# Kernel tuning notes

Measured on AMD Instinct MI355X. Metric: run time of the kernel, lower is better.

The kernel has to match this reference:

```python
import jax, jax.numpy as jnp
import numpy as np

N = 100000
NFEAT = 128
NHID = 16
HEADS = 8
NCLASS = 40
E = 1600000
NEG_SLOPE = 0.2  # PyG GATConv default


def glorot(key, shape):
    fan = shape[0] + shape[-1]
    limit = float(np.sqrt(6.0 / fan))
    return jax.random.uniform(key, shape, jnp.float32, -limit, limit)


def setup_inputs() -> dict:
    key = jax.random.key(0)
    ks = jax.random.split(key, 10)
    x = jax.random.normal(ks[0], (N, NFEAT), jnp.float32)
    adj = jnp.zeros((1,), jnp.float32)  # unused by forward, kept for signature parity
    edge_index = jax.random.randint(ks[1], (2, E), 0, N, jnp.int64)
    # layer 1: GATConv(NFEAT, NHID, heads=HEADS)
    W1 = glorot(ks[2], (NFEAT, HEADS * NHID))
    att_src1 = glorot(ks[3], (HEADS, NHID))
    att_dst1 = glorot(ks[4], (HEADS, NHID))
    b1 = jnp.zeros((HEADS * NHID,), jnp.float32)
    # layer 2: GATConv(HEADS*NHID, NCLASS, heads=1)
    W2 = glorot(ks[5], (HEADS * NHID, NCLASS))
    att_src2 = glorot(ks[6], (1, NCLASS))
    att_dst2 = glorot(ks[7], (1, NCLASS))
    b2 = jnp.zeros((NCLASS,), jnp.float32)
    return {"x": x, "adj": adj, "edge_index": edge_index,
            "W1": W1, "att_src1": att_src1, "att_dst1": att_dst1, "b1": b1,
            "W2": W2, "att_src2": att_src2, "att_dst2": att_dst2, "b2": b2}


def gat_conv(x, W, att_src, att_dst, bias, src, dst, heads, out_ch):
    n = x.shape[0]
    h = (x @ W).reshape(n, heads, out_ch)              # [N,H,C]
    a_src = (h * att_src[None]).sum(-1)                # [N,H]
    a_dst = (h * att_dst[None]).sum(-1)                # [N,H]
    e = jax.nn.leaky_relu(a_src[src] + a_dst[dst], NEG_SLOPE)  # [E,H]
    # softmax over incoming edges of each destination node
    m = jax.ops.segment_max(e, dst, num_segments=n)
    e = jnp.exp(e - m[dst])
    s = jax.ops.segment_sum(e, dst, num_segments=n)
    alpha = e / s[dst]                                  # [E,H]
    msg = h[src] * alpha[:, :, None]                    # [E,H,C]
    out = jax.ops.segment_sum(msg, dst, num_segments=n)  # [N,H,C]
    return out.reshape(n, heads * out_ch) + bias


def reference(x, adj, edge_index, W1, att_src1, att_dst1, b1, W2, att_src2, att_dst2, b2):
    # PyG GATConv adds self-loops by default
    loops = jnp.arange(N, dtype=edge_index.dtype)
    src = jnp.concatenate([edge_index[0], loops])
    dst = jnp.concatenate([edge_index[1], loops])
    # eval mode: F.dropout is identity
    h = jax.nn.elu(gat_conv(x, W1, att_src1, att_dst1, b1, src, dst, HEADS, NHID))
    h = jax.nn.elu(gat_conv(h, W2, att_src2, att_dst2, b2, src, dst, 1, NCLASS))
    return jax.nn.log_softmax(h, axis=1)
```

## Files before the change

kernel.cpp:

```cpp
#include <hip/hip_runtime.h>
#include <stdint.h>

#define NEG_SLOPE 0.2f

__device__ __forceinline__ float lrelu(float v) { return v >= 0.f ? v : NEG_SLOPE * v; }
__device__ __forceinline__ float elu(float v) { return v > 0.f ? v : expm1f(v); }
__device__ __forceinline__ float pexp(float v) { return __expf(lrelu(v)); }

typedef _Float16 h16x2 __attribute__((ext_vector_type(2)));
typedef _Float16 half8 __attribute__((ext_vector_type(8)));
typedef float floatx4 __attribute__((ext_vector_type(4)));

__device__ __forceinline__ void fma_h2(float& a0, float& a1, float p, unsigned u) {
    h16x2 h = __builtin_bit_cast(h16x2, u);
    a0 += p * (float)h[0];
    a1 += p * (float)h[1];
}


__global__ void zero_deg_kernel(int* __restrict__ deg, int n) {
    int t = blockIdx.x * blockDim.x + threadIdx.x;
    if (t < n) deg[t] = 0;
}

__global__ void hist_kernel(const int* __restrict__ ei, int* __restrict__ deg,
                            int* __restrict__ rank, int E, int n) {
    int e = blockIdx.x * blockDim.x + threadIdx.x;
    if (e >= E) return;
    int s = ei[e], d = ei[E + e];
    int r = -1;
    if ((unsigned)s < (unsigned)n && (unsigned)d < (unsigned)n)
        r = atomicAdd(&deg[d], 1);
    rank[e] = r;
}

#define SCAN_T 256
#define SCAN_TILE 1024

__global__ __launch_bounds__(SCAN_T) void scan_p1_kernel(const int* __restrict__ deg,
                                                         int* __restrict__ bsum, int n) {
    __shared__ int red[SCAN_T];
    int t = threadIdx.x;
    int base = blockIdx.x * SCAN_TILE + t * 4;
    int s = 0;
    #pragma unroll
    for (int i = 0; i < 4; i++) {
        int idx = base + i;
        if (idx < n) s += deg[idx];
    }
    red[t] = s;
    __syncthreads();
    for (int off = SCAN_T / 2; off; off >>= 1) {
        if (t < off) red[t] += red[t + off];
        __syncthreads();
    }
    if (t == 0) bsum[blockIdx.x] = red[0];
}

__global__ __launch_bounds__(1024) void scan_p2_kernel(int* __restrict__ bsum, int nb,
                                                       int* __restrict__ total) {
    __shared__ int sh[1024];
    int t = threadIdx.x;
    int v = (t < nb) ? bsum[t] : 0;
    sh[t] = v;
    __syncthreads();
    for (int off = 1; off < 1024; off <<= 1) {
        int add = (t >= off) ? sh[t - off] : 0;
        __syncthreads();
        sh[t] += add;
        __syncthreads();
    }
    if (t < nb) bsum[t] = sh[t] - v;
    if (t == nb - 1) *total = sh[t];
}

__global__ __launch_bounds__(SCAN_T) void scan_p3_kernel(const int* __restrict__ deg,
                                                         const int* __restrict__ bsum,
                                                         int* __restrict__ row_ptr, int n) {
    __shared__ int red[SCAN_T];
    int t = threadIdx.x;
    int base = blockIdx.x * SCAN_TILE + t * 4;
    int v[4];
    int s = 0;
    #pragma unroll
    for (int i = 0; i < 4; i++) {
        int idx = base + i;
        v[i] = (idx < n) ? deg[idx] : 0;
        s += v[i];
    }
    red[t] = s;
    __syncthreads();
    for (int off = 1; off < SCAN_T; off <<= 1) {
        int add = (t >= off) ? red[t - off] : 0;
        __syncthreads();
        red[t] += add;
        __syncthreads();
    }
    int excl = red[t] - s + bsum[blockIdx.x];
    #pragma unroll
    for (int i = 0; i < 4; i++) {
        int idx = base + i;
        if (idx < n) row_ptr[idx] = excl;
        excl += v[i];
    }
}

__global__ void scatter_kernel(const int* __restrict__ ei, const int* __restrict__ rank,
                               const int* __restrict__ row_ptr,
                               int* __restrict__ csr_src, int E, int n) {
    int e = blockIdx.x * blockDim.x + threadIdx.x;
    if (e >= E) return;
    int r = rank[e];
    if (r < 0) return;
    int s = ei[e], d = ei[E + e];
    csr_src[row_ptr[d] + r] = s;
}


__global__ void w1t_kernel(const float* __restrict__ W1, _Float16* __restrict__ w1t) {
    int t = blockIdx.x * 256 + threadIdx.x;
    int col = t >> 7, k = t & 127;
    w1t[col * 128 + k] = (_Float16)W1[k * 128 + col];
}

__global__ __launch_bounds__(256) void gemm1_mfma_kernel(
    const float* __restrict__ x, const _Float16* __restrict__ w1t,
    const float* __restrict__ as1, const float* __restrict__ ad1,
    _Float16* __restrict__ h1h, float* __restrict__ a1s, float* __restrict__ a1d, int n) {
    __shared__ __align__(16) char Wl[32768];
    const int tid = threadIdx.x;
    {
        const uint4* Wg = (const uint4*)w1t;
        #pragma unroll
        for (int i = 0; i < 8; i++) {
            int it = tid + i * 256;
            uint4 v = Wg[it];
            int b = it * 16;
            *(uint4*)&Wl[b ^ (((b >> 8) & 7) << 4)] = v;
        }
    }
    const int wave = tid >> 6, lane = tid & 63;
    const int cl = lane & 15, g = lane >> 4;
    const int wbase = blockIdx.x * 64 + wave * 16;

    int arow = wbase + cl;
    if (arow >= n) arow = n - 1;
    half8 afr[4];
    #pragma unroll
    for (int t = 0; t < 4; t++) {
        const float4 v0 = *(const float4*)&x[(size_t)arow * 128 + 32 * t + g * 8];
        const float4 v1 = *(const float4*)&x[(size_t)arow * 128 + 32 * t + g * 8 + 4];
        afr[t][0] = (_Float16)v0.x; afr[t][1] = (_Float16)v0.y;
        afr[t][2] = (_Float16)v0.z; afr[t][3] = (_Float16)v0.w;
        afr[t][4] = (_Float16)v1.x; afr[t][5] = (_Float16)v1.y;
        afr[t][6] = (_Float16)v1.z; afr[t][7] = (_Float16)v1.w;
    }
    __syncthreads();

    #pragma unroll
    for (int ct = 0; ct < 8; ct++) {
        const int col = ct * 16 + cl;
        half8 bfr[4];
        #pragma unroll
        for (int t = 0; t < 4; t++) {
            int b = (col << 8) + 64 * t + 16 * g;
            bfr[t] = *(half8*)&Wl[b ^ ((col & 7) << 4)];
        }
        floatx4 acc = {0.f, 0.f, 0.f, 0.f};
        #pragma unroll
        for (int t = 0; t < 4; t++)
            acc = __builtin_amdgcn_mfma_f32_16x16x32_f16(afr[t], bfr[t], acc, 0, 0, 0);
        const float av = as1[col], dv = ad1[col];
        #pragma unroll
        for (int i = 0; i < 4; i++) {
            int r = wbase + g * 4 + i;
            float hv = acc[i];
            if (r < n) h1h[(size_t)r * 128 + col] = (_Float16)hv;
            float ps = hv * av, pd = hv * dv;
            ps += __shfl_xor(ps, 1); ps += __shfl_xor(ps, 2);
            ps += __shfl_xor(ps, 4); ps += __shfl_xor(ps, 8);
            pd += __shfl_xor(pd, 1); pd += __shfl_xor(pd, 2);
            pd += __shfl_xor(pd, 4); pd += __shfl_xor(pd, 8);
            if (cl == 0 && r < n) {
                a1s[r * 8 + ct] = ps;
                a1d[r * 8 + ct] = pd;
            }
        }
    }
}

__global__ __launch_bounds__(256) void agg1_kernel(const int* __restrict__ row_ptr,
                                                   const int* __restrict__ csr_src,
                                                   const float* __restrict__ a1s,
                                                   const float* __restrict__ a1d,
                                                   const uint4* __restrict__ h1q,
                                                   const float* __restrict__ b1,
                                                   float* __restrict__ h2, int n) {
    int lane = threadIdx.x & 63;
    int d = blockIdx.x * 4 + (threadIdx.x >> 6);
    if (d >= n) return;
    const int g = lane >> 4;
    const int q = lane & 15;
    const int h = q >> 1;
    const float adh = a1d[d * 8 + h];

    float acc[8];
    #pragma unroll
    for (int i = 0; i < 8; i++) acc[i] = 0.f;
    float sum = 0.f;
    if (g == 0) {
        uint4 w = h1q[(size_t)d * 16 + q];
        float ps = pexp(a1s[d * 8 + h] + adh);
        fma_h2(acc[0], acc[1], ps, w.x);
        fma_h2(acc[2], acc[3], ps, w.y);
        fma_h2(acc[4], acc[5], ps, w.z);
        fma_h2(acc[6], acc[7], ps, w.w);
        sum = ps;
    }
    int beg = row_ptr[d], end = row_ptr[d + 1];
    for (int e = beg + g; e < end; e += 4) {
        int s = csr_src[e];
        uint4 w = h1q[(size_t)s * 16 + q];
        float p = pexp(a1s[s * 8 + h] + adh);
        fma_h2(acc[0], acc[1], p, w.x);
        fma_h2(acc[2], acc[3], p, w.y);
        fma_h2(acc[4], acc[5], p, w.z);
        fma_h2(acc[6], acc[7], p, w.w);
        sum += p;
    }
    sum += __shfl_xor(sum, 16); sum += __shfl_xor(sum, 32);
    #pragma unroll
    for (int i = 0; i < 8; i++) {
        acc[i] += __shfl_xor(acc[i], 16);
        acc[i] += __shfl_xor(acc[i], 32);
    }
    if (g == 0) {
        float rs = 1.f / sum;
        float4 b0 = *(const float4*)&b1[8 * q];
        float4 b4 = *(const float4*)&b1[8 * q + 4];
        float4 o0, o1;
        o0.x = elu(acc[0] * rs + b0.x); o0.y = elu(acc[1] * rs + b0.y);
        o0.z = elu(acc[2] * rs + b0.z); o0.w = elu(acc[3] * rs + b0.w);
        o1.x = elu(acc[4] * rs + b4.x); o1.y = elu(acc[5] * rs + b4.y);
        o1.z = elu(acc[6] * rs + b4.z); o1.w = elu(acc[7] * rs + b4.w);
        *(float4*)&h2[(size_t)d * 128 + 8 * q] = o0;
        *(float4*)&h2[(size_t)d * 128 + 8 * q + 4] = o1;
    }
}


#define WT_STRIDE 136
__global__ __launch_bounds__(320, 4) void gemm2_kernel(const float* __restrict__ h2,
                                                       const float* __restrict__ W2,
                                                       float* __restrict__ h3f,
                                                       _Float16* __restrict__ h3h,
                                                       int n) {
    __shared__ float WsT[40 * WT_STRIDE];
    __shared__ float xs[64][128];
    const int tid = threadIdx.x;
    const int j = tid % 40;
    const int no = tid / 40;
    const int base = blockIdx.x * 64;

    #pragma unroll 1
    for (int i = tid; i < 128 * 40; i += 320) {
        int k = i / 40, jj = i % 40;
        WsT[jj * WT_STRIDE + k] = W2[i];
    }
    #pragma unroll 1
    for (int q = tid; q < 64 * 32; q += 320) {
        int nn = q >> 5, c4 = q & 31;
        int node = base + nn;
        float4 v = make_float4(0.f, 0.f, 0.f, 0.f);
        if (node < n) v = *(const float4*)&h2[(size_t)node * 128 + c4 * 4];
        *(float4*)&xs[nn][c4 * 4] = v;
    }
    __syncthreads();

    float acc[8];
    #pragma unroll
    for (int m = 0; m < 8; m++) acc[m] = 0.f;
    #pragma unroll 4
    for (int k4 = 0; k4 < 128; k4 += 4) {
        float4 wv = *(const float4*)&WsT[j * WT_STRIDE + k4];
        #pragma unroll
        for (int m = 0; m < 8; m++) {
            float4 xv = *(const float4*)&xs[no + m * 8][k4];
            acc[m] += xv.x * wv.x + xv.y * wv.y + xv.z * wv.z + xv.w * wv.w;
        }
    }
    #pragma unroll
    for (int m = 0; m < 8; m++) {
        int node = base + no + m * 8;
        if (node < n) {
            h3f[(size_t)node * 40 + j] = acc[m];
            h3h[(size_t)node * 40 + j] = (_Float16)acc[m];
        }
    }
}

__global__ void attn2_kernel(const float* __restrict__ h3f, const float* __restrict__ as2,
                             const float* __restrict__ ad2,
                             float* __restrict__ a2s, float* __restrict__ a2d, int n) {
    int t = blockIdx.x * blockDim.x + threadIdx.x;
    if (t >= n) return;
    const float* row = &h3f[(size_t)t * 40];
    float ss = 0.f, dd = 0.f;
    #pragma unroll
    for (int c = 0; c < 40; c++) {
        float v = row[c];
        ss += v * as2[c];
        dd += v * ad2[c];
    }
    a2s[t] = ss;
    a2d[t] = dd;
}

__global__ __launch_bounds__(256) void agg2_final_kernel(const int* __restrict__ row_ptr,
                                                         const int* __restrict__ csr_src,
                                                         const float* __restrict__ a2s,
                                                         const float* __restrict__ a2d,
                                                         const float* __restrict__ h3f,
                                                         const unsigned* __restrict__ h3p,
                                                         const float* __restrict__ b2,
                                                         float* __restrict__ out, int n) {
    int lane = threadIdx.x & 63;
    int d = blockIdx.x * 4 + (threadIdx.x >> 6);
    if (d >= n) return;
    const int g = lane >> 5;
    const int q = lane & 31;
    const bool act = (q < 20);

    float2 hv = make_float2(0.f, 0.f);
    if (act && g == 0) hv = *(const float2*)&h3f[(size_t)d * 40 + 2 * q];
    const float adh = a2d[d];

    float acc0 = 0.f, acc1 = 0.f, sum = 0.f;
    if (g == 0) {
        float ps = pexp(a2s[d] + adh);
        acc0 = ps * hv.x; acc1 = ps * hv.y; sum = ps;
    }
    int beg = row_ptr[d], end = row_ptr[d + 1];
    int e = beg + g;
    for (; e + 6 < end; e += 8) {
        int s0 = csr_src[e],     s1 = csr_src[e + 2];
        int s2 = csr_src[e + 4], s3 = csr_src[e + 6];
        float a0 = a2s[s0], a1 = a2s[s1], a2 = a2s[s2], a3 = a2s[s3];
        unsigned w0 = 0u, w1 = 0u, w2 = 0u, w3 = 0u;
        if (act) {
            w0 = h3p[(size_t)s0 * 20 + q]; w1 = h3p[(size_t)s1 * 20 + q];
            w2 = h3p[(size_t)s2 * 20 + q]; w3 = h3p[(size_t)s3 * 20 + q];
        }
        float p0 = pexp(a0 + adh), p1 = pexp(a1 + adh);
        float p2 = pexp(a2 + adh), p3 = pexp(a3 + adh);
        fma_h2(acc0, acc1, p0, w0);
        fma_h2(acc0, acc1, p1, w1);
        fma_h2(acc0, acc1, p2, w2);
        fma_h2(acc0, acc1, p3, w3);
        sum += (p0 + p1) + (p2 + p3);
    }
    for (; e < end; e += 2) {
        int s = csr_src[e];
        float pe = pexp(a2s[s] + adh);
        unsigned w = act ? h3p[(size_t)s * 20 + q] : 0u;
        fma_h2(acc0, acc1, pe, w);
        sum += pe;
    }
    sum += __shfl_xor(sum, 32);
    acc0 += __shfl_xor(acc0, 32);
    acc1 += __shfl_xor(acc1, 32);

    float rs = 1.f / sum;
    float v0 = -3.0e38f, v1 = -3.0e38f;
    if (act) {
        v0 = elu(acc0 * rs + b2[2 * q]);
        v1 = elu(acc1 * rs + b2[2 * q + 1]);
    }
    float mx = (act && g == 0) ? fmaxf(v0, v1) : -3.0e38f;
    #pragma unroll
    for (int off = 32; off; off >>= 1) mx = fmaxf(mx, __shfl_xor(mx, off, 64));
    float es = (act && g == 0) ? (__expf(v0 - mx) + __expf(v1 - mx)) : 0.f;
    #pragma unroll
    for (int off = 32; off; off >>= 1) es += __shfl_xor(es, off, 64);
    if (act && g == 0) {
        float ls = logf(es);
        float2 o;
        o.x = v0 - mx - ls;
        o.y = v1 - mx - ls;
        *(float2*)&out[(size_t)d * 40 + 2 * q] = o;
    }
}

extern "C" void kernel_launch(void* const* d_in, const int* in_sizes, int n_in,
                              void* d_out, int out_size, void* d_ws, size_t ws_size,
                              hipStream_t stream) {
    const float* x   = (const float*)d_in[0];
    const int*   ei  = (const int*)d_in[2];
    const float* W1  = (const float*)d_in[3];
    const float* as1 = (const float*)d_in[4];
    const float* ad1 = (const float*)d_in[5];
    const float* b1  = (const float*)d_in[6];
    const float* W2  = (const float*)d_in[7];
    const float* as2 = (const float*)d_in[8];
    const float* ad2 = (const float*)d_in[9];
    const float* b2  = (const float*)d_in[10];
    float* out = (float*)d_out;

    const int n = in_sizes[0] / 128;
    const int E = in_sizes[2] / 2;
    const int nb = (n + SCAN_TILE - 1) / SCAN_TILE;

    float* ws = (float*)d_ws;
    _Float16* h1h = (_Float16*)ws;
    float* h2 = ws + (size_t)n * 64;
    float* A  = h2 + (size_t)n * 128;
    int* deg    = (int*)A;
    int* bsum   = deg + n;
    float* a1s  = A;
    float* a1d  = A + (size_t)n * 8;
    float* a2s  = A;
    float* a2d  = A + (size_t)n;
    int* row_ptr = (int*)(A + (size_t)n * 16);
    int* csr_src = row_ptr + (n + 1);
    int* rank    = csr_src + E;
    _Float16* w1t = (_Float16*)(((uintptr_t)(rank + E) + 63) & ~(uintptr_t)63);
    _Float16* h3h = h1h;
    float* h3f = ws + (size_t)n * 20;

    w1t_kernel<<<64, 256, 0, stream>>>(W1, w1t);
    zero_deg_kernel<<<(n + 255) / 256, 256, 0, stream>>>(deg, n);
    hist_kernel<<<(E + 255) / 256, 256, 0, stream>>>(ei, deg, rank, E, n);
    scan_p1_kernel<<<nb, SCAN_T, 0, stream>>>(deg, bsum, n);
    scan_p2_kernel<<<1, 1024, 0, stream>>>(bsum, nb, &row_ptr[n]);
    scan_p3_kernel<<<nb, SCAN_T, 0, stream>>>(deg, bsum, row_ptr, n);
    scatter_kernel<<<(E + 255) / 256, 256, 0, stream>>>(ei, rank, row_ptr, csr_src, E, n);

    gemm1_mfma_kernel<<<(n + 63) / 64, 256, 0, stream>>>(x, w1t, as1, ad1, h1h, a1s, a1d, n);
    agg1_kernel<<<(n + 3) / 4, 256, 0, stream>>>(row_ptr, csr_src, a1s, a1d,
                                                 (const uint4*)h1h, b1, h2, n);

    gemm2_kernel<<<(n + 63) / 64, 320, 0, stream>>>(h2, W2, h3f, h3h, n);
    attn2_kernel<<<(n + 255) / 256, 256, 0, stream>>>(h3f, as2, ad2, a2s, a2d, n);
    agg2_final_kernel<<<(n + 3) / 4, 256, 0, stream>>>(row_ptr, csr_src, a2s, a2d, h3f,
                                                       (const unsigned*)h3h, b2, out, n);
}
```

Before: 485.5 us.

## Use fp16 MFMA for layer-2 GEMM, fuse attention scores, store h2 as fp16

Layer-1 aggregation now writes its ELU output as fp16 instead of fp32. Layer 2 then runs its projection with 16x16x32 f16 MFMA instructions against a pre-transposed, zero-padded fp16 W2, and computes the attention source and destination scores in the same kernel, which removes the separate attn2 pass. The agg1 edge loop is also unrolled by two to keep more gathers in flight. The aim is to cut h2 memory traffic and FP32 FMA cost in gemm2, at the price of fp16 rounding of the layer-2 input.

Result: faster. 419.3 us (-13.6%).

```diff
diff --git a/kernel.cpp b/kernel.cpp
--- a/kernel.cpp
+++ b/kernel.cpp
@@ -122,6 +122,14 @@
     int col = t >> 7, k = t & 127;
     w1t[col * 128 + k] = (_Float16)W1[k * 128 + col];
 }
+
+__global__ void w2t_kernel(const float* __restrict__ W2, _Float16* __restrict__ w2t) {
+    int t = blockIdx.x * 256 + threadIdx.x;
+    if (t >= 48 * 128) return;
+    int col = t >> 7, k = t & 127;
+    w2t[t] = (col < 40) ? (_Float16)W2[k * 40 + col] : (_Float16)0.f;
+}
+
 
 __global__ __launch_bounds__(256) void gemm1_mfma_kernel(
     const float* __restrict__ x, const _Float16* __restrict__ w1t,
@@ -195,7 +203,7 @@
                                                    const float* __restrict__ a1d,
                                                    const uint4* __restrict__ h1q,
                                                    const float* __restrict__ b1,
-                                                   float* __restrict__ h2, int n) {
+                                                   _Float16* __restrict__ h2h, int n) {
     int lane = threadIdx.x & 63;
     int d = blockIdx.x * 4 + (threadIdx.x >> 6);
     if (d >= n) return;
@@ -218,7 +226,24 @@
         sum = ps;
     }
     int beg = row_ptr[d], end = row_ptr[d + 1];
-    for (int e = beg + g; e < end; e += 4) {
+    int e = beg + g;
+    for (; e + 4 < end; e += 8) {
+        int s0 = csr_src[e], s1 = csr_src[e + 4];
+        uint4 w0 = h1q[(size_t)s0 * 16 + q];
+        uint4 w1 = h1q[(size_t)s1 * 16 + q];
+        float p0 = pexp(a1s[s0 * 8 + h] + adh);
+        float p1 = pexp(a1s[s1 * 8 + h] + adh);
+        fma_h2(acc[0], acc[1], p0, w0.x);
+        fma_h2(acc[2], acc[3], p0, w0.y);
+        fma_h2(acc[4], acc[5], p0, w0.z);
+        fma_h2(acc[6], acc[7], p0, w0.w);
+        fma_h2(acc[0], acc[1], p1, w1.x);
+        fma_h2(acc[2], acc[3], p1, w1.y);
+        fma_h2(acc[4], acc[5], p1, w1.z);
+        fma_h2(acc[6], acc[7], p1, w1.w);
+        sum += p0 + p1;
+    }
+    for (; e < end; e += 4) {
         int s = csr_src[e];
         uint4 w = h1q[(size_t)s * 16 + q];
         float p = pexp(a1s[s * 8 + h] + adh);
@@ -238,82 +263,78 @@
         float rs = 1.f / sum;
         float4 b0 = *(const float4*)&b1[8 * q];
         float4 b4 = *(const float4*)&b1[8 * q + 4];
-        float4 o0, o1;
-        o0.x = elu(acc[0] * rs + b0.x); o0.y = elu(acc[1] * rs + b0.y);
-        o0.z = elu(acc[2] * rs + b0.z); o0.w = elu(acc[3] * rs + b0.w);
-        o1.x = elu(acc[4] * rs + b4.x); o1.y = elu(acc[5] * rs + b4.y);
-        o1.z = elu(acc[6] * rs + b4.z); o1.w = elu(acc[7] * rs + b4.w);
-        *(float4*)&h2[(size_t)d * 128 + 8 * q] = o0;
-        *(float4*)&h2[(size_t)d * 128 + 8 * q + 4] = o1;
-    }
-}
-
-
-#define WT_STRIDE 136
-__global__ __launch_bounds__(320, 4) void gemm2_kernel(const float* __restrict__ h2,
-                                                       const float* __restrict__ W2,
-                                                       float* __restrict__ h3f,
-                                                       _Float16* __restrict__ h3h,
-                                                       int n) {
-    __shared__ float WsT[40 * WT_STRIDE];
-    __shared__ float xs[64][128];
+        half8 o;
+        o[0] = (_Float16)elu(acc[0] * rs + b0.x);
+        o[1] = (_Float16)elu(acc[1] * rs + b0.y);
+        o[2] = (_Float16)elu(acc[2] * rs + b0.z);
+        o[3] = (_Float16)elu(acc[3] * rs + b0.w);
+        o[4] = (_Float16)elu(acc[4] * rs + b4.x);
+        o[5] = (_Float16)elu(acc[5] * rs + b4.y);
+        o[6] = (_Float16)elu(acc[6] * rs + b4.z);
+        o[7] = (_Float16)elu(acc[7] * rs + b4.w);
+        *(half8*)&h2h[(size_t)d * 128 + 8 * q] = o;
+    }
+}
+
+
+__global__ __launch_bounds__(256) void gemm2_mfma_kernel(
+    const _Float16* __restrict__ h2h, const _Float16* __restrict__ w2t,
+    const float* __restrict__ as2, const float* __restrict__ ad2,
+    float* __restrict__ h3f, _Float16* __restrict__ h3h,
+    float* __restrict__ a2s, float* __restrict__ a2d, int n) {
     const int tid = threadIdx.x;
-    const int j = tid % 40;
-    const int no = tid / 40;
-    const int base = blockIdx.x * 64;
-
-    #pragma unroll 1
-    for (int i = tid; i < 128 * 40; i += 320) {
-        int k = i / 40, jj = i % 40;
-        WsT[jj * WT_STRIDE + k] = W2[i];
-    }
-    #pragma unroll 1
-    for (int q = tid; q < 64 * 32; q += 320) {
-        int nn = q >> 5, c4 = q & 31;
-        int node = base + nn;
-        float4 v = make_float4(0.f, 0.f, 0.f, 0.f);
-        if (node < n) v = *(const float4*)&h2[(size_t)node * 128 + c4 * 4];
-        *(float4*)&xs[nn][c4 * 4] = v;
-    }
-    __syncthreads();
-
-    float acc[8];
-    #pragma unroll
-    for (int m = 0; m < 8; m++) acc[m] = 0.f;
-    #pragma unroll 4
-    for (int k4 = 0; k4 < 128; k4 += 4) {
-        float4 wv = *(const float4*)&WsT[j * WT_STRIDE + k4];
-        #pragma unroll
-        for (int m = 0; m < 8; m++) {
-            float4 xv = *(const float4*)&xs[no + m * 8][k4];
-            acc[m] += xv.x * wv.x + xv.y * wv.y + xv.z * wv.z + xv.w * wv.w;
-        }
-    }
-    #pragma unroll
-    for (int m = 0; m < 8; m++) {
-        int node = base + no + m * 8;
-        if (node < n) {
-            h3f[(size_t)node * 40 + j] = acc[m];
-            h3h[(size_t)node * 40 + j] = (_Float16)acc[m];
-        }
-    }
-}
-
-__global__ void attn2_kernel(const float* __restrict__ h3f, const float* __restrict__ as2,
-                             const float* __restrict__ ad2,
-                             float* __restrict__ a2s, float* __restrict__ a2d, int n) {
-    int t = blockIdx.x * blockDim.x + threadIdx.x;
-    if (t >= n) return;
-    const float* row = &h3f[(size_t)t * 40];
-    float ss = 0.f, dd = 0.f;
-    #pragma unroll
-    for (int c = 0; c < 40; c++) {
-        float v = row[c];
-        ss += v * as2[c];
-        dd += v * ad2[c];
-    }
-    a2s[t] = ss;
-    a2d[t] = dd;
+    const int wave = tid >> 6, lane = tid & 63;
+    const int cl = lane & 15, g = lane >> 4;
+    const int wbase = blockIdx.x * 64 + wave * 16;
+
+    int arow = wbase + cl;
+    if (arow >= n) arow = n - 1;
+    half8 afr[4];
+    #pragma unroll
+    for (int t = 0; t < 4; t++)
+        afr[t] = *(const half8*)&h2h[(size_t)arow * 128 + 32 * t + 8 * g];
+
+    float ps[4] = {0.f, 0.f, 0.f, 0.f};
+    float pd[4] = {0.f, 0.f, 0.f, 0.f};
+    #pragma unroll
+    for (int ct = 0; ct < 3; ct++) {
+        const int col = ct * 16 + cl;
+        half8 bfr[4];
+        #pragma unroll
+        for (int t = 0; t < 4; t++)
+            bfr[t] = *(const half8*)&w2t[col * 128 + 32 * t + 8 * g];
+        floatx4 acc = {0.f, 0.f, 0.f, 0.f};
+        #pragma unroll
+        for (int t = 0; t < 4; t++)
+            acc = __builtin_amdgcn_mfma_f32_16x16x32_f16(afr[t], bfr[t], acc, 0, 0, 0);
+        const bool cv = (col < 40);
+        const float av = cv ? as2[col] : 0.f;
+        const float dv = cv ? ad2[col] : 0.f;
+        #pragma unroll
+        for (int i = 0; i < 4; i++) {
+            int r = wbase + g * 4 + i;
+            float hv = acc[i];
+            if (cv && r < n) {
+                h3f[(size_t)r * 40 + col] = hv;
+                h3h[(size_t)r * 40 + col] = (_Float16)hv;
+            }
+            ps[i] += hv * av;
+            pd[i] += hv * dv;
+        }
+    }
+    #pragma unroll
+    for (int i = 0; i < 4; i++) {
+        float s = ps[i], dd = pd[i];
+        s += __shfl_xor(s, 1); s += __shfl_xor(s, 2);
+        s += __shfl_xor(s, 4); s += __shfl_xor(s, 8);
+        dd += __shfl_xor(dd, 1); dd += __shfl_xor(dd, 2);
+        dd += __shfl_xor(dd, 4); dd += __shfl_xor(dd, 8);
+        int r = wbase + g * 4 + i;
+        if (cl == 0 && r < n) {
+            a2s[r] = s;
+            a2d[r] = dd;
+        }
+    }
 }
 
 __global__ __launch_bounds__(256) void agg2_final_kernel(const int* __restrict__ row_ptr,
@@ -412,8 +433,8 @@
 
     float* ws = (float*)d_ws;
     _Float16* h1h = (_Float16*)ws;
-    float* h2 = ws + (size_t)n * 64;
-    float* A  = h2 + (size_t)n * 128;
+    _Float16* h2h = (_Float16*)(ws + (size_t)n * 64);
+    float* A  = ws + (size_t)n * 128;
     int* deg    = (int*)A;
     int* bsum   = deg + n;
     float* a1s  = A;
@@ -424,10 +445,12 @@
     int* csr_src = row_ptr + (n + 1);
     int* rank    = csr_src + E;
     _Float16* w1t = (_Float16*)(((uintptr_t)(rank + E) + 63) & ~(uintptr_t)63);
+    _Float16* w2t = w1t + 128 * 128;
     _Float16* h3h = h1h;
     float* h3f = ws + (size_t)n * 20;
 
     w1t_kernel<<<64, 256, 0, stream>>>(W1, w1t);
+    w2t_kernel<<<24, 256, 0, stream>>>(W2, w2t);
     zero_deg_kernel<<<(n + 255) / 256, 256, 0, stream>>>(deg, n);
     hist_kernel<<<(E + 255) / 256, 256, 0, stream>>>(ei, deg, rank, E, n);
     scan_p1_kernel<<<nb, SCAN_T, 0, stream>>>(deg, bsum, n);
@@ -437,10 +460,10 @@
 
     gemm1_mfma_kernel<<<(n + 63) / 64, 256, 0, stream>>>(x, w1t, as1, ad1, h1h, a1s, a1d, n);
     agg1_kernel<<<(n + 3) / 4, 256, 0, stream>>>(row_ptr, csr_src, a1s, a1d,
-                                                 (const uint4*)h1h, b1, h2, n);
-
-    gemm2_kernel<<<(n + 63) / 64, 320, 0, stream>>>(h2, W2, h3f, h3h, n);
-    attn2_kernel<<<(n + 255) / 256, 256, 0, stream>>>(h3f, as2, ad2, a2s, a2d, n);
+                                                 (const uint4*)h1h, b1, h2h, n);
+
+    gemm2_mfma_kernel<<<(n + 63) / 64, 256, 0, stream>>>(h2h, w2t, as2, ad2,
+                                                         h3f, h3h, a2s, a2d, n);
     agg2_final_kernel<<<(n + 3) / 4, 256, 0, stream>>>(row_ptr, csr_src, a2s, a2d, h3f,
                                                        (const unsigned*)h3h, b2, out, n);
 }
```
